# Kernel optimization log

Hardware: AMD Instinct MI355X
Metric: run time of the kernel (lower is better)

The kernel has to match this reference:

```python
import jax, jax.numpy as jnp
import numpy as np

CLASSES = 21
IOU_THRESH = 0.5
ALPHA, GAMMA = 0.25, 2.0
CLS_W, REG_W = 1.0, 1.0


def _make_boxes(key, shape):
    # valid xyxy boxes: x1<x2, y1<y2 inside unit square
    k1, k2 = jax.random.split(key)
    xy1 = jax.random.uniform(k1, shape[:-1] + (2,)) * 0.8
    wh = jax.random.uniform(k2, shape[:-1] + (2,)) * 0.19 + 0.01
    return jnp.concatenate([xy1, xy1 + wh], axis=-1).astype(jnp.float32)


def setup_inputs() -> dict:
    key = jax.random.key(0)
    k1, k2, k3, k4, k5 = jax.random.split(key, 5)
    B, A, T = 4, 49152, 50
    return {
        "classification_preds": jax.random.normal(k1, (B, A, CLASSES), dtype=jnp.float32),
        "boxes_preds": _make_boxes(k2, (B, A, 4)),
        "anchors": _make_boxes(k3, (B, A, 4)),
        "target_boxes": _make_boxes(k4, (B, T, 4)),
        "target_labels": jax.random.randint(k5, (B, T), 1, CLASSES),  # 1..20 (0=background)
    }


def compute_iou(a, b):
    # a: [T,4] xyxy, b: [A,4] xyxy -> [T,A]
    lt = jnp.maximum(a[:, None, :2], b[None, :, :2])
    rb = jnp.minimum(a[:, None, 2:], b[None, :, 2:])
    wh = jnp.clip(rb - lt, 0.0)
    inter = wh[..., 0] * wh[..., 1]
    area_a = (a[:, 2] - a[:, 0]) * (a[:, 3] - a[:, 1])
    area_b = (b[:, 2] - b[:, 0]) * (b[:, 3] - b[:, 1])
    union = area_a[:, None] + area_b[None, :] - inter
    return inter / jnp.clip(union, 1e-8)


def encode(boxes, anchors):
    # xyxy -> center offsets relative to anchors
    bc = (boxes[:, :2] + boxes[:, 2:]) * 0.5
    bwh = boxes[:, 2:] - boxes[:, :2]
    ac = (anchors[:, :2] + anchors[:, 2:]) * 0.5
    awh = anchors[:, 2:] - anchors[:, :2]
    txy = (bc - ac) / awh
    twh = jnp.log(bwh / awh)
    return jnp.concatenate([txy, twh], axis=-1)


def focal_loss(logits, targets):
    p = jax.nn.sigmoid(logits)
    ce = -(targets * jax.nn.log_sigmoid(logits) + (1.0 - targets) * jax.nn.log_sigmoid(-logits))
    pt = targets * p + (1.0 - targets) * (1.0 - p)
    alpha_t = targets * ALPHA + (1.0 - targets) * (1.0 - ALPHA)
    return alpha_t * (1.0 - pt) ** GAMMA * ce


def smooth_l1(x, y):
    d = jnp.abs(x - y)
    return jnp.where(d < 1.0, 0.5 * d * d, d - 0.5)


def reference(classification_preds, boxes_preds, anchors, target_boxes, target_labels):
    cls = classification_preds.reshape(-1, CLASSES)   # [A, C]
    box = boxes_preds.reshape(-1, 4)                  # [A, 4]
    anc = anchors.reshape(-1, 4)                      # [A, 4]
    tb = target_boxes.reshape(-1, 4)                  # [T, 4]
    tl = target_labels.reshape(-1)                    # [T]

    iou = compute_iou(tb, anc)                        # [T, A]
    max_iou = jnp.max(iou, axis=0)                    # [A]
    tid = jnp.argmax(iou, axis=0)                     # [A]
    pos = max_iou >= IOU_THRESH                       # [A]
    pos_cnt = jnp.sum(pos.astype(jnp.int32))
    norm = jnp.clip(pos_cnt, 1).astype(cls.dtype)

    onehot = jax.nn.one_hot(tl[tid], CLASSES, dtype=cls.dtype)        # [A, C]
    background = jax.nn.one_hot(0, CLASSES, dtype=cls.dtype)          # [C]
    cls_tgt = jnp.where(pos[:, None], onehot, background[None, :])    # [A, C]

    cls_loss = jnp.sum(focal_loss(cls, cls_tgt)) / norm

    enc_pred = encode(box, anc)                       # [A, 4]
    enc_tgt = encode(tb[tid], anc)                    # [A, 4]
    reg_elem = smooth_l1(enc_pred, enc_tgt) * pos[:, None].astype(cls.dtype)
    reg_loss = jnp.sum(reg_elem) / (norm * 4.0)       # mean over positive elements
    reg_loss = jnp.where(pos_cnt > 0, reg_loss, 0.0)

    wc = cls_loss * CLS_W
    wr = reg_loss * REG_W
    return (wc + wr, wc, wr)
```

## Files before the change

### kernel.cpp

```cpp
#include <hip/hip_runtime.h>
#include <hip/hip_bf16.h>


#define CLASSES 21
#define TPB 256
#define APB 64
#define MAXT 256

__global__ __launch_bounds__(TPB, 8)
void main_kernel(const float* __restrict__ cls,
                 const float4* __restrict__ box,
                 const float4* __restrict__ anc,
                 const int* __restrict__ labels,
                 const float4* __restrict__ tbox,
                 float* __restrict__ pc,
                 float* __restrict__ pr,
                 float* __restrict__ pp,
                 int A, int T) {
    __shared__ float4 s_tb[MAXT];

    int tid = threadIdx.x;
    for (int t = tid; t < T; t += TPB) {
        s_tb[t] = tbox[t];
    }
    __syncthreads();

    int p = tid & 3;
    int a = blockIdx.x * APB + (tid >> 2);

    float cls_p = 0.0f, reg_p = 0.0f, pos_p = 0.0f;
    float ax1 = 0.f, ay1 = 0.f, ax2 = 0.f, ay2 = 0.f;
    float bI = 0.0f, bU = 1.0f;
    int bT = 0;

    if (a < A) {
        float4 av = anc[a];
        ax1 = av.x; ay1 = av.y; ax2 = av.z; ay2 = av.w;
        float areaA = (ax2 - ax1) * (ay2 - ay1);

        #pragma unroll 2
        for (int t = p; t < T; t += 4) {
            float4 tv = s_tb[t];
            float ta = (tv.z - tv.x) * (tv.w - tv.y);
            float lx = fmaxf(tv.x, ax1);
            float ly = fmaxf(tv.y, ay1);
            float rx = fminf(tv.z, ax2);
            float ry = fminf(tv.w, ay2);
            float w = fmaxf(rx - lx, 0.0f);
            float h = fmaxf(ry - ly, 0.0f);
            float inter = w * h;
            float uni = (ta + areaA) - inter;
            bool gt = inter * bU > bI * uni;
            bI = gt ? inter : bI;
            bU = gt ? uni : bU;
            bT = gt ? t : bT;
        }
    }

    #pragma unroll
    for (int d = 1; d <= 2; d <<= 1) {
        float oI = __shfl_xor(bI, d, 64);
        float oU = __shfl_xor(bU, d, 64);
        int   oT = __shfl_xor(bT, d, 64);
        bool gt = oI * bU > bI * oU;
        bI = gt ? oI : bI;
        bU = gt ? oU : bU;
        bT = gt ? oT : bT;
    }

    if (a < A) {
        bool pos = (bI + bI) >= bU;

        int hot = pos ? labels[bT] : 0;
        const float* crow = cls + (size_t)a * CLASSES;
        float csum = 0.0f;
        #pragma unroll
        for (int k = 0; k < 6; ++k) {
            int j = p + 4 * k;
            if (j < CLASSES) {
                float x = crow[j];
                float y = (j == hot) ? -x : x;
                float em = __expf(-fabsf(y));
                float sp = fmaxf(y, 0.0f) + __logf(1.0f + em);
                float r1 = __builtin_amdgcn_rcpf(1.0f + em);
                float sg = (y >= 0.0f) ? r1 : em * r1;
                float f = sg * sg * sp;
                csum = fmaf(f, (j == hot) ? (1.0f / 3.0f) : 1.0f, csum);
            }
        }
        cls_p = csum * 0.75f;

        if (pos && p == 0) {
            pos_p = 1.0f;
            float4 bv = box[a];
            float4 tv = s_tb[bT];
            float aw = ax2 - ax1, ah = ay2 - ay1;
            float acx = (ax1 + ax2) * 0.5f, acy = (ay1 + ay2) * 0.5f;
            float ep0 = ((bv.x + bv.z) * 0.5f - acx) / aw;
            float ep1 = ((bv.y + bv.w) * 0.5f - acy) / ah;
            float ep2 = __logf((bv.z - bv.x) / aw);
            float ep3 = __logf((bv.w - bv.y) / ah);
            float et0 = ((tv.x + tv.z) * 0.5f - acx) / aw;
            float et1 = ((tv.y + tv.w) * 0.5f - acy) / ah;
            float et2 = __logf((tv.z - tv.x) / aw);
            float et3 = __logf((tv.w - tv.y) / ah);
            float r = 0.0f, d;
            d = fabsf(ep0 - et0); r += (d < 1.0f) ? 0.5f * d * d : d - 0.5f;
            d = fabsf(ep1 - et1); r += (d < 1.0f) ? 0.5f * d * d : d - 0.5f;
            d = fabsf(ep2 - et2); r += (d < 1.0f) ? 0.5f * d * d : d - 0.5f;
            d = fabsf(ep3 - et3); r += (d < 1.0f) ? 0.5f * d * d : d - 0.5f;
            reg_p = r;
        }
    }

    #pragma unroll
    for (int off = 32; off > 0; off >>= 1) {
        cls_p += __shfl_down(cls_p, off, 64);
        reg_p += __shfl_down(reg_p, off, 64);
        pos_p += __shfl_down(pos_p, off, 64);
    }
    __shared__ float red[3][TPB / 64];
    int wave = tid >> 6;
    int lane = tid & 63;
    if (lane == 0) {
        red[0][wave] = cls_p;
        red[1][wave] = reg_p;
        red[2][wave] = pos_p;
    }
    __syncthreads();
    if (tid == 0) {
        float c = 0.0f, r = 0.0f, q = 0.0f;
        #pragma unroll
        for (int wv = 0; wv < TPB / 64; ++wv) {
            c += red[0][wv]; r += red[1][wv]; q += red[2][wv];
        }
        pc[blockIdx.x] = c;
        pr[blockIdx.x] = r;
        pp[blockIdx.x] = q;
    }
}

__global__ __launch_bounds__(TPB)
void fin_kernel(const float* __restrict__ pc,
                const float* __restrict__ pr,
                const float* __restrict__ pp,
                int nb, float* __restrict__ out) {
    int tid = threadIdx.x;
    float c = 0.0f, r = 0.0f, q = 0.0f;
    for (int i = tid; i < nb; i += TPB) {
        c += pc[i]; r += pr[i]; q += pp[i];
    }
    #pragma unroll
    for (int off = 32; off > 0; off >>= 1) {
        c += __shfl_down(c, off, 64);
        r += __shfl_down(r, off, 64);
        q += __shfl_down(q, off, 64);
    }
    __shared__ float red[3][TPB / 64];
    int wave = tid >> 6;
    int lane = tid & 63;
    if (lane == 0) { red[0][wave] = c; red[1][wave] = r; red[2][wave] = q; }
    __syncthreads();
    if (tid == 0) {
        float cs = 0.0f, rs = 0.0f, qs = 0.0f;
        #pragma unroll
        for (int wv = 0; wv < TPB / 64; ++wv) {
            cs += red[0][wv]; rs += red[1][wv]; qs += red[2][wv];
        }
        float norm = fmaxf(qs, 1.0f);
        float wc = cs / norm;
        float wr = (qs > 0.0f) ? rs / (norm * 4.0f) : 0.0f;
        out[0] = wc + wr;
        out[1] = wc;
        out[2] = wr;
    }
}

extern "C" void kernel_launch(void* const* d_in, const int* in_sizes, int n_in,
                              void* d_out, int out_size, void* d_ws, size_t ws_size,
                              hipStream_t stream) {
    const float* cls  = (const float*)d_in[0];
    const float4* box = (const float4*)d_in[1];
    const float4* anc = (const float4*)d_in[2];
    const float4* tb  = (const float4*)d_in[3];
    const int* tl     = (const int*)d_in[4];

    int A = in_sizes[0] / CLASSES;
    int T = in_sizes[4];

    int nb = (A + APB - 1) / APB;
    float* pc = (float*)d_ws;
    float* pr = pc + nb;
    float* pp = pr + nb;

    main_kernel<<<nb, TPB, 0, stream>>>(cls, box, anc, tl, tb, pc, pr, pp, A, T);
    fin_kernel<<<1, TPB, 0, stream>>>(pc, pr, pp, nb, (float*)d_out);
}
```

Measured before the change: 105.5 us.

## Split IoU matching into chunked kernel and stage class logits through LDS

Replaces the single fused kernel with a four-launch pipeline. A prep kernel precomputes target areas. A chunked IoU kernel splits targets into four groups per anchor and writes partial best matches to workspace, and a loss kernel merges those partials, stages each block's class logits into shared memory with float4 copies, and computes focal and regression loss with one thread per anchor. This aims to improve parallelism and coalescing, but adds extra launches, round-trips of partial results through global memory, and a large shared-memory footprint (about 21 KB per block) that may limit occupancy.

```diff
diff --git a/kernel.cpp b/kernel.cpp
--- a/kernel.cpp
+++ b/kernel.cpp
@@ -1,101 +1,129 @@
 #include <hip/hip_runtime.h>
-#include <hip/hip_bf16.h>
 
 
 #define CLASSES 21
 #define TPB 256
-#define APB 64
-#define MAXT 256
-
-__global__ __launch_bounds__(TPB, 8)
-void main_kernel(const float* __restrict__ cls,
+#define G 4
+
+__global__ void prep_kernel(const float4* __restrict__ tb,
+                            float* __restrict__ tarea, int T) {
+    int t = blockIdx.x * blockDim.x + threadIdx.x;
+    if (t < T) {
+        float4 v = tb[t];
+        tarea[t] = (v.z - v.x) * (v.w - v.y);
+    }
+}
+
+__global__ __launch_bounds__(TPB)
+void iou_kernel(const float4* __restrict__ anc,
+                const float4* __restrict__ tbox,
+                const float* __restrict__ tarea,
+                float* __restrict__ pbI, float* __restrict__ pbU,
+                int* __restrict__ pbT,
+                int A, int T, int chunk) {
+    int c  = blockIdx.x & (G - 1);
+    int ab = blockIdx.x >> 2;
+    int a  = ab * TPB + threadIdx.x;
+    if (a >= A) return;
+
+    float4 av = anc[a];
+    float areaA = (av.z - av.x) * (av.w - av.y);
+
+    int t0 = c * chunk;
+    int t1 = min(T, t0 + chunk);
+    float bI = 0.0f, bU = 1.0f;
+    int bT = t0;
+    #pragma unroll 10
+    for (int t = t0; t < t1; ++t) {
+        float4 tv = tbox[t];
+        float ta = tarea[t];
+        float lx = fmaxf(tv.x, av.x);
+        float ly = fmaxf(tv.y, av.y);
+        float rx = fminf(tv.z, av.z);
+        float ry = fminf(tv.w, av.w);
+        float w = fmaxf(rx - lx, 0.0f);
+        float h = fmaxf(ry - ly, 0.0f);
+        float inter = w * h;
+        float uni = (ta + areaA) - inter;
+        bool gt = inter * bU > bI * uni;
+        bI = gt ? inter : bI;
+        bU = gt ? uni : bU;
+        bT = gt ? t : bT;
+    }
+    size_t o = (size_t)c * A + a;
+    pbI[o] = bI;
+    pbU[o] = bU;
+    pbT[o] = bT;
+}
+
+__global__ __launch_bounds__(TPB)
+void loss_kernel(const float* __restrict__ cls,
                  const float4* __restrict__ box,
                  const float4* __restrict__ anc,
                  const int* __restrict__ labels,
                  const float4* __restrict__ tbox,
-                 float* __restrict__ pc,
-                 float* __restrict__ pr,
+                 const float* __restrict__ pbI, const float* __restrict__ pbU,
+                 const int* __restrict__ pbT,
+                 float* __restrict__ pc, float* __restrict__ pr,
                  float* __restrict__ pp,
-                 int A, int T) {
-    __shared__ float4 s_tb[MAXT];
-
+                 int A) {
+    __shared__ float s_cls[TPB * CLASSES];
     int tid = threadIdx.x;
-    for (int t = tid; t < T; t += TPB) {
-        s_tb[t] = tbox[t];
+    int a = blockIdx.x * TPB + tid;
+
+    {
+        const float4* g4 = (const float4*)(cls + (size_t)blockIdx.x * TPB * CLASSES);
+        float4* s4 = (float4*)s_cls;
+        int n4 = (TPB * CLASSES) / 4;
+        int lim4 = min(n4, (int)(((size_t)A * CLASSES - (size_t)blockIdx.x * TPB * CLASSES) / 4));
+        for (int i = tid; i < lim4; i += TPB) s4[i] = g4[i];
     }
     __syncthreads();
 
-    int p = tid & 3;
-    int a = blockIdx.x * APB + (tid >> 2);
-
     float cls_p = 0.0f, reg_p = 0.0f, pos_p = 0.0f;
-    float ax1 = 0.f, ay1 = 0.f, ax2 = 0.f, ay2 = 0.f;
-    float bI = 0.0f, bU = 1.0f;
-    int bT = 0;
 
     if (a < A) {
-        float4 av = anc[a];
-        ax1 = av.x; ay1 = av.y; ax2 = av.z; ay2 = av.w;
-        float areaA = (ax2 - ax1) * (ay2 - ay1);
-
-        #pragma unroll 2
-        for (int t = p; t < T; t += 4) {
-            float4 tv = s_tb[t];
-            float ta = (tv.z - tv.x) * (tv.w - tv.y);
-            float lx = fmaxf(tv.x, ax1);
-            float ly = fmaxf(tv.y, ay1);
-            float rx = fminf(tv.z, ax2);
-            float ry = fminf(tv.w, ay2);
-            float w = fmaxf(rx - lx, 0.0f);
-            float h = fmaxf(ry - ly, 0.0f);
-            float inter = w * h;
-            float uni = (ta + areaA) - inter;
-            bool gt = inter * bU > bI * uni;
-            bI = gt ? inter : bI;
-            bU = gt ? uni : bU;
-            bT = gt ? t : bT;
-        }
-    }
-
-    #pragma unroll
-    for (int d = 1; d <= 2; d <<= 1) {
-        float oI = __shfl_xor(bI, d, 64);
-        float oU = __shfl_xor(bU, d, 64);
-        int   oT = __shfl_xor(bT, d, 64);
-        bool gt = oI * bU > bI * oU;
-        bI = gt ? oI : bI;
-        bU = gt ? oU : bU;
-        bT = gt ? oT : bT;
-    }
-
-    if (a < A) {
+        float bI = 0.0f, bU = 1.0f;
+        int bT = 0;
+        #pragma unroll
+        for (int c = 0; c < G; ++c) {
+            size_t o = (size_t)c * A + a;
+            float oI = pbI[o];
+            float oU = pbU[o];
+            int   oT = pbT[o];
+            if (c == 0) { bI = oI; bU = oU; bT = oT; }
+            else {
+                bool gt = oI * bU > bI * oU;
+                bI = gt ? oI : bI;
+                bU = gt ? oU : bU;
+                bT = gt ? oT : bT;
+            }
+        }
         bool pos = (bI + bI) >= bU;
 
         int hot = pos ? labels[bT] : 0;
-        const float* crow = cls + (size_t)a * CLASSES;
+        const float* crow = s_cls + tid * CLASSES;
         float csum = 0.0f;
         #pragma unroll
-        for (int k = 0; k < 6; ++k) {
-            int j = p + 4 * k;
-            if (j < CLASSES) {
-                float x = crow[j];
-                float y = (j == hot) ? -x : x;
-                float em = __expf(-fabsf(y));
-                float sp = fmaxf(y, 0.0f) + __logf(1.0f + em);
-                float r1 = __builtin_amdgcn_rcpf(1.0f + em);
-                float sg = (y >= 0.0f) ? r1 : em * r1;
-                float f = sg * sg * sp;
-                csum = fmaf(f, (j == hot) ? (1.0f / 3.0f) : 1.0f, csum);
-            }
+        for (int j = 0; j < CLASSES; ++j) {
+            float x = crow[j];
+            float y = (j == hot) ? -x : x;
+            float em = __expf(-fabsf(y));
+            float sp = fmaxf(y, 0.0f) + __logf(1.0f + em);
+            float r1 = __builtin_amdgcn_rcpf(1.0f + em);
+            float sg = (y >= 0.0f) ? r1 : em * r1;
+            float f = sg * sg * sp;
+            csum = fmaf(f, (j == hot) ? (1.0f / 3.0f) : 1.0f, csum);
         }
         cls_p = csum * 0.75f;
 
-        if (pos && p == 0) {
+        if (pos) {
             pos_p = 1.0f;
+            float4 av = anc[a];
             float4 bv = box[a];
-            float4 tv = s_tb[bT];
-            float aw = ax2 - ax1, ah = ay2 - ay1;
-            float acx = (ax1 + ax2) * 0.5f, acy = (ay1 + ay2) * 0.5f;
+            float4 tv = tbox[bT];
+            float aw = av.z - av.x, ah = av.w - av.y;
+            float acx = (av.x + av.z) * 0.5f, acy = (av.y + av.w) * 0.5f;
             float ep0 = ((bv.x + bv.z) * 0.5f - acx) / aw;
             float ep1 = ((bv.y + bv.w) * 0.5f - acy) / ah;
             float ep2 = __logf((bv.z - bv.x) / aw);
@@ -187,12 +215,24 @@
 
     int A = in_sizes[0] / CLASSES;
     int T = in_sizes[4];
-
-    int nb = (A + APB - 1) / APB;
-    float* pc = (float*)d_ws;
-    float* pr = pc + nb;
-    float* pp = pr + nb;
-
-    main_kernel<<<nb, TPB, 0, stream>>>(cls, box, anc, tl, tb, pc, pr, pp, A, T);
-    fin_kernel<<<1, TPB, 0, stream>>>(pc, pr, pp, nb, (float*)d_out);
-}
+    int chunk = (T + G - 1) / G;
+
+    float* tarea = (float*)d_ws;
+    float* pbI   = (float*)((char*)d_ws + 4096);
+    float* pbU   = pbI + (size_t)G * A;
+    int*   pbT   = (int*)(pbU + (size_t)G * A);
+    int nb2 = (A + TPB - 1) / TPB;
+    float* pc = (float*)(pbT + (size_t)G * A);
+    float* pr = pc + nb2;
+    float* pp = pr + nb2;
+
+    prep_kernel<<<(T + TPB - 1) / TPB, TPB, 0, stream>>>(tb, tarea, T);
+
+    int nb1 = nb2 * G;
+    iou_kernel<<<nb1, TPB, 0, stream>>>(anc, tb, tarea, pbI, pbU, pbT, A, T, chunk);
+
+    loss_kernel<<<nb2, TPB, 0, stream>>>(cls, box, anc, tl, tb,
+                                         pbI, pbU, pbT, pc, pr, pp, A);
+
+    fin_kernel<<<1, TPB, 0, stream>>>(pc, pr, pp, nb2, (float*)d_out);
+}
```

New measurement: 104.4 us. About the same (-1.1%).
